# Kernel tuning notes

Hardware: AMD Instinct MI355X
Metric: run time of the kernel (lower is better)

The kernel has to match this reference:

```python
import jax, jax.numpy as jnp
import numpy as np

N_NODES = 10000
N_EDGES = 160000
INPUT_DIM = 24
HIDDEN = 256
Z_DIM = 32
OUT_DIM = 24
HEADS = 2
EW = 2
ENC = HIDDEN + OUT_DIM + 256          # 536
DEC = Z_DIM + HIDDEN + 256            # 544
ENC2 = ENC * HEADS                    # 1072
DEC2 = DEC * HEADS                    # 1088
ENC_MLP_IN = ENC2 + OUT_DIM           # 1096
DEC_MLP_IN = DEC2 + Z_DIM             # 1120


def _lin(key, o, i):
    # kaiming-ish scaling so attention logits stay numerically sane
    return (jax.random.normal(key, (o, i), jnp.float32) / np.sqrt(i)).astype(jnp.float32)


def setup_inputs() -> dict:
    key = jax.random.key(0)
    ks = jax.random.split(key, 32)
    inp = {
        'feats': jax.random.normal(ks[0], (N_NODES, INPUT_DIM), jnp.float32),
        'gt': jax.random.normal(ks[1], (N_NODES, OUT_DIM), jnp.float32),
        'maps_emb': jax.random.normal(ks[2], (N_NODES, 256), jnp.float32),
        'e_w': jax.random.uniform(ks[3], (N_EDGES, EW), jnp.float32),
        'eps': jax.random.normal(ks[4], (N_NODES, Z_DIM), jnp.float32),
        'src': jax.random.randint(ks[5], (N_EDGES,), 0, N_NODES, jnp.int32),
        'dst': jax.random.randint(ks[6], (N_EDGES,), 0, N_NODES, jnp.int32),
        # embedding_h
        'emb_W': _lin(ks[7], HIDDEN, INPUT_DIM),
        'emb_b': jnp.zeros((HIDDEN,), jnp.float32),
        # encoder GAT layer 1 (2 heads, att_ew: Wa covers [z_src|z_dst|ew])
        'enc1_Ws': jnp.stack([_lin(ks[8], ENC, ENC), _lin(ks[9], ENC, ENC)]),
        'enc1_Wf': jnp.stack([_lin(ks[10], ENC, ENC), _lin(ks[11], ENC, ENC)]),
        'enc1_Wa': jnp.stack([_lin(ks[12], 1, 3 * ENC)[0], _lin(ks[13], 1, 3 * ENC)[0]]),
        # encoder GAT layer 2 (1 head, att_ew)
        'enc2_Ws': _lin(ks[14], ENC2, ENC2),
        'enc2_Wf': _lin(ks[15], ENC2, ENC2),
        'enc2_Wa': _lin(ks[16], 1, 3 * ENC2)[0],
        # MLP encoder
        'encmlp_W': _lin(ks[17], ENC_MLP_IN // 2, ENC_MLP_IN),
        'encmlp_b': jnp.zeros((ENC_MLP_IN // 2,), jnp.float32),
        'mu_W': _lin(ks[18], Z_DIM, ENC_MLP_IN // 2),
        'mu_b': jnp.zeros((Z_DIM,), jnp.float32),
        'lv_W': _lin(ks[19], Z_DIM, ENC_MLP_IN // 2),
        'lv_b': jnp.zeros((Z_DIM,), jnp.float32),
        # decoder GAT layer 1 (2 heads, no edge weights in attention)
        'dec1_Ws': jnp.stack([_lin(ks[20], DEC, DEC), _lin(ks[21], DEC, DEC)]),
        'dec1_Wf': jnp.stack([_lin(ks[22], DEC, DEC), _lin(ks[23], DEC, DEC)]),
        'dec1_Wa': jnp.stack([_lin(ks[24], 1, 2 * DEC)[0], _lin(ks[25], 1, 2 * DEC)[0]]),
        # decoder GAT layer 2 (1 head)
        'dec2_Ws': _lin(ks[26], DEC2, DEC2),
        'dec2_Wf': _lin(ks[27], DEC2, DEC2),
        'dec2_Wa': _lin(ks[28], 1, 2 * DEC2)[0],
        # MLP decoder
        'dec0_W': _lin(ks[29], DEC, DEC_MLP_IN),
        'dec0_b': jnp.zeros((DEC,), jnp.float32),
        'dec1o_W': _lin(ks[30], OUT_DIM, DEC),
        'dec1o_b': jnp.zeros((OUT_DIM,), jnp.float32),
    }
    return inp


def rep_pad(ew, pad):
    # nn.ReplicationPad1d(pad): replicate first/last edge-weight column
    left = jnp.repeat(ew[:, :1], pad, axis=1)
    right = jnp.repeat(ew[:, -1:], pad, axis=1)
    return jnp.concatenate([left, ew, right], axis=1)


def gat(h, Ws, Wf, Wa, ew, src, dst, n):
    """One My_GATLayer head: self-lin + gather-attn-softmax-aggregate + relu + residual."""
    out = Ws.shape[0]
    h_s = h @ Ws.T                       # [n, out]
    z = h @ Wf.T                         # [n, out]
    # attention logits without materializing concat([z_src, z_dst, ew])
    logit = (z @ Wa[:out])[src] + (z @ Wa[out:2 * out])[dst]
    if Wa.shape[0] > 2 * out:
        logit = logit + ew @ Wa[2 * out:]
    e = jax.nn.leaky_relu(logit, 0.01)   # [E]
    # per-destination-node edge softmax
    m = jax.ops.segment_max(e, dst, num_segments=n)
    m = jnp.where(jnp.isfinite(m), m, 0.0)
    ex = jnp.exp(e - m[dst])
    s = jax.ops.segment_sum(ex, dst, num_segments=n)
    alpha = ex / s[dst]
    agg = jax.ops.segment_sum(alpha[:, None] * z[src], dst, num_segments=n)
    deg = jax.ops.segment_sum(jnp.ones_like(ex), dst, num_segments=n)
    # DGL: zero-in-degree nodes keep their pre-update ndata['h'] (the input h)
    hn = jnp.where(deg[:, None] > 0, h_s + agg, h)
    return h + jnp.maximum(hn, 0.0)      # relu=True, res_connection=True


def reference(feats, gt, maps_emb, e_w, eps,
              emb_W, emb_b,
              enc1_Ws, enc1_Wf, enc1_Wa, enc2_Ws, enc2_Wf, enc2_Wa,
              encmlp_W, encmlp_b, mu_W, mu_b, lv_W, lv_b,
              dec1_Ws, dec1_Wf, dec1_Wa, dec2_Ws, dec2_Wf, dec2_Wa,
              dec0_W, dec0_b, dec1o_W, dec1o_b,
              src, dst):
    n = feats.shape[0]
    h_emb = feats @ emb_W.T + emb_b
    # ---------------- encoder GAT-VAE ----------------
    h = jnp.concatenate([maps_emb, h_emb, gt], axis=-1)        # [n, ENC]
    e1 = rep_pad(e_w, h.shape[-1] // 2 - 1)                    # [E, ENC]
    h = jnp.concatenate(
        [gat(h, enc1_Ws[i], enc1_Wf[i], enc1_Wa[i], e1, src, dst, n)
         for i in range(enc1_Ws.shape[0])], axis=1)            # [n, ENC*heads]
    e2 = rep_pad(e_w, h.shape[-1] // 2 - 1)                    # [E, ENC*heads]
    h = gat(h, enc2_Ws, enc2_Wf, enc2_Wa, e2, src, dst, n)
    # ---------------- MLP encoder + reparameterize ----------------
    he = jnp.concatenate([h, gt], axis=-1)
    he = jax.nn.leaky_relu(he @ encmlp_W.T + encmlp_b, 0.01)
    mu = he @ mu_W.T + mu_b
    log_var = he @ lv_W.T + lv_b
    z = mu + jnp.exp(0.5 * log_var) * eps
    # ---------------- decoder GAT-VAE (att_ew=False) ----------------
    hd = jnp.concatenate([maps_emb, h_emb, z], axis=-1)        # [n, DEC]
    hd = jnp.concatenate(
        [gat(hd, dec1_Ws[i], dec1_Wf[i], dec1_Wa[i], None, src, dst, n)
         for i in range(dec1_Ws.shape[0])], axis=1)            # [n, DEC*heads]
    hd = gat(hd, dec2_Ws, dec2_Wf, dec2_Wa, None, src, dst, n)
    # ---------------- MLP decoder ----------------
    hd = jnp.concatenate([hd, z], axis=-1)
    hd = jax.nn.leaky_relu(hd @ dec0_W.T + dec0_b, 0.02)
    recon_y = hd @ dec1o_W.T + dec1o_b
    return recon_y
```

## Files before the change

kernel.cpp:

```cpp
#include <hip/hip_runtime.h>
#include <hip/hip_bf16.h>
#include <hip/hip_fp16.h>

#define N_NODES 10000
#define N_EDGES 160000

typedef __attribute__((ext_vector_type(8))) short bf16x8;
typedef __attribute__((ext_vector_type(4))) float f32x4;
typedef __attribute__((ext_vector_type(4))) unsigned short us4v;
typedef unsigned short ushort_t;

__device__ __forceinline__ ushort_t f2bf(float x) {
    union { float f; unsigned u; } c; c.f = x;
    unsigned u = c.u;
    u += 0x7fffu + ((u >> 16) & 1u);
    return (ushort_t)(u >> 16);
}
__device__ __forceinline__ float bf2f(ushort_t b) {
    union { unsigned u; float f; } c; c.u = ((unsigned)b) << 16;
    return c.f;
}
__device__ __forceinline__ ushort_t f2h(float x) {
    return __half_as_ushort(__float2half(x));
}
__device__ __forceinline__ float h2f(ushort_t h) {
    return __half2float(__ushort_as_half(h));
}

__global__ __launch_bounds__(256) void k_split(
    const float* __restrict__ src, int R, int K, int Kp,
    ushort_t* __restrict__ oh, ushort_t* __restrict__ ol, int row_off)
{
    const int q = Kp >> 2;
    const int idx = blockIdx.x * 256 + threadIdx.x;
    if (idx >= R * q) return;
    const int r = idx / q;
    const int k = (idx - r * q) << 2;
    float4 v = make_float4(0.f, 0.f, 0.f, 0.f);
    if (k < K) v = *reinterpret_cast<const float4*>(&src[(size_t)r * K + k]);
    float vv[4] = {v.x, v.y, v.z, v.w};
    us4v h, l;
    #pragma unroll
    for (int j = 0; j < 4; ++j) {
        const ushort_t hb = f2bf(vv[j]);
        h[j] = hb;
        l[j] = f2bf(vv[j] - bf2f(hb));
    }
    const size_t o = (size_t)(r + row_off) * Kp + k;
    *reinterpret_cast<us4v*>(&oh[o]) = h;
    *reinterpret_cast<us4v*>(&ol[o]) = l;
}

__global__ __launch_bounds__(256) void k_mgemm(
    const ushort_t* __restrict__ Ah, const ushort_t* __restrict__ Al,
    const ushort_t* __restrict__ Wh, const ushort_t* __restrict__ Wl,
    const float* __restrict__ bias0, const float* __restrict__ bias1,
    float* __restrict__ C0, int ld0, int M1,
    float* __restrict__ C1, int ld1,
    ushort_t* __restrict__ Z16, int ld16,
    int Nr, int Kp, int Mc, int act, float slope)
{
    __shared__ ushort_t As[128 * 64];
    __shared__ ushort_t Bs[128 * 64];

    const int tid = threadIdx.x;
    const int w = tid >> 6, l = tid & 63;
    const int wr = w >> 1, wc = w & 1;
    const int row0 = blockIdx.y * 128, col0 = blockIdx.x * 128;

    const int rsub = l >> 3;
    const int cg = (((l & 7) ^ (rsub & 7)) << 3);
    const int fr = l & 15, fq = l >> 4;
    const int ca0 = (((0 * 4 + fq) ^ (l & 7)) << 3);
    const int ca1 = (((1 * 4 + fq) ^ (l & 7)) << 3);

    f32x4 acc[4][4];
    #pragma unroll
    for (int m = 0; m < 4; ++m)
        #pragma unroll
        for (int n = 0; n < 4; ++n)
            acc[m][n] = {0.f, 0.f, 0.f, 0.f};

    auto run_seg = [&](const ushort_t* __restrict__ pa,
                       const ushort_t* __restrict__ pb) {
        for (int kt = 0; kt < Kp; kt += 64) {
            #pragma unroll
            for (int i = 0; i < 4; ++i) {
                const int r = w * 32 + i * 8 + rsub;
                int gra = row0 + r; gra = gra < Nr ? gra : Nr - 1;
                const ushort_t* ga = pa + (size_t)gra * Kp + kt + cg;
                __builtin_amdgcn_global_load_lds(
                    (const __attribute__((address_space(1))) void*)ga,
                    (__attribute__((address_space(3))) void*)&As[(w * 32 + i * 8) * 64],
                    16, 0, 0);
                int grb = col0 + r; grb = grb < Mc ? grb : Mc - 1;
                const ushort_t* gb = pb + (size_t)grb * Kp + kt + cg;
                __builtin_amdgcn_global_load_lds(
                    (const __attribute__((address_space(1))) void*)gb,
                    (__attribute__((address_space(3))) void*)&Bs[(w * 32 + i * 8) * 64],
                    16, 0, 0);
            }
            __syncthreads();
            #pragma unroll
            for (int ks = 0; ks < 2; ++ks) {
                const int ca = ks ? ca1 : ca0;
                bf16x8 af[4], bf[4];
                #pragma unroll
                for (int m = 0; m < 4; ++m)
                    af[m] = *reinterpret_cast<const bf16x8*>(
                        &As[(wr * 64 + m * 16 + fr) * 64 + ca]);
                #pragma unroll
                for (int n = 0; n < 4; ++n)
                    bf[n] = *reinterpret_cast<const bf16x8*>(
                        &Bs[(wc * 64 + n * 16 + fr) * 64 + ca]);
                #pragma unroll
                for (int m = 0; m < 4; ++m)
                    #pragma unroll
                    for (int n = 0; n < 4; ++n)
                        acc[m][n] = __builtin_amdgcn_mfma_f32_16x16x32_bf16(
                            af[m], bf[n], acc[m][n], 0, 0, 0);
            }
            __syncthreads();
        }
    };

    run_seg(Ah, Wh);
    run_seg(Ah, Wl);
    run_seg(Al, Wh);

    #pragma unroll
    for (int n = 0; n < 4; ++n) {
        const int col = col0 + wc * 64 + n * 16 + fr;
        if (col >= Mc) continue;
        float bv = 0.f;
        if (col < M1) { if (bias0) bv = bias0[col]; }
        else          { if (bias1) bv = bias1[col - M1]; }
        #pragma unroll
        for (int m = 0; m < 4; ++m) {
            #pragma unroll
            for (int r = 0; r < 4; ++r) {
                const int row = row0 + wr * 64 + m * 16 + fq * 4 + r;
                if (row >= Nr) continue;
                float v = acc[m][n][r] + bv;
                if (act) v = v >= 0.f ? v : v * slope;
                if (col < M1) {
                    if (Z16) Z16[(size_t)row * ld16 + col] = f2h(v);
                    else     C0[(size_t)row * ld0 + col] = v;
                } else {
                    C1[(size_t)row * ld1 + (col - M1)] = v;
                }
            }
        }
    }
}

__global__ void k_hist(const int* __restrict__ dst, int E, int* __restrict__ cnt)
{
    const int e = blockIdx.x * blockDim.x + threadIdx.x;
    if (e < E) atomicAdd(&cnt[dst[e]], 1);
}

__global__ __launch_bounds__(256) void k_scan(const int* __restrict__ cnt,
                                              int* __restrict__ rs, int n)
{
    __shared__ int sums[256];
    const int tid = threadIdx.x;
    const int T = (n + 255) / 256;
    const int base = tid * T;
    int s = 0;
    for (int i = 0; i < T; ++i) { const int idx = base + i; if (idx < n) s += cnt[idx]; }
    sums[tid] = s;
    __syncthreads();
    for (int o = 1; o < 256; o <<= 1) {
        const int v = (tid >= o) ? sums[tid - o] : 0;
        __syncthreads();
        sums[tid] += v;
        __syncthreads();
    }
    int run = (tid == 0) ? 0 : sums[tid - 1];
    for (int i = 0; i < T; ++i) {
        const int idx = base + i;
        if (idx < n) { rs[idx] = run; run += cnt[idx]; }
    }
    if (tid == 255) rs[n] = sums[255];
}

__global__ void k_fill(const int* __restrict__ src, const int* __restrict__ dst,
                       const float* __restrict__ ew, int E,
                       const int* __restrict__ rs, int* __restrict__ cur,
                       int* __restrict__ csrc, float* __restrict__ cew0,
                       float* __restrict__ cew1)
{
    const int e = blockIdx.x * blockDim.x + threadIdx.x;
    if (e >= E) return;
    const int d = dst[e];
    const int pos = rs[d] + atomicAdd(&cur[d], 1);
    csrc[pos] = src[e];
    cew0[pos] = ew[2 * e];
    cew1[pos] = ew[2 * e + 1];
}

__global__ __launch_bounds__(256) void k_dotwa(
    const ushort_t* __restrict__ Z16, const float* __restrict__ wa, int K, int N,
    float* __restrict__ za_s, float* __restrict__ za_d)
{
    const int lane = threadIdx.x & 63;
    const int node = blockIdx.x * 4 + (threadIdx.x >> 6);
    if (node >= N) return;
    const ushort_t* zr = Z16 + (size_t)node * K;
    float s = 0.f, d = 0.f;
    for (int k = lane; k < K; k += 64) {
        const float zv = h2f(zr[k]);
        s += zv * wa[k];
        d += zv * wa[K + k];
    }
    #pragma unroll
    for (int o = 32; o; o >>= 1) { s += __shfl_xor(s, o); d += __shfl_xor(d, o); }
    if (lane == 0) { za_s[node] = s; za_d[node] = d; }
}

__global__ __launch_bounds__(256) void k_wasums(const float* __restrict__ wa,
                                                int out, float* __restrict__ sums)
{
    __shared__ float red[256];
    const int tid = threadIdx.x;
    const int half = out >> 1;
    const float* t0 = wa + 2 * out;
    float s0 = 0.f, s1 = 0.f;
    for (int i = tid; i < half; i += 256) { s0 += t0[i]; s1 += t0[half + i]; }
    red[tid] = s0; __syncthreads();
    for (int o = 128; o; o >>= 1) { if (tid < o) red[tid] += red[tid + o]; __syncthreads(); }
    if (tid == 0) sums[0] = red[0];
    __syncthreads();
    red[tid] = s1; __syncthreads();
    for (int o = 128; o; o >>= 1) { if (tid < o) red[tid] += red[tid + o]; __syncthreads(); }
    if (tid == 0) sums[1] = red[0];
}

__global__ __launch_bounds__(256) void k_attn(
    const int* __restrict__ rs, const int* __restrict__ csrc,
    const float* __restrict__ cew0, const float* __restrict__ cew1,
    const float* __restrict__ za_s, const float* __restrict__ za_d,
    const float* __restrict__ ewsums, float* __restrict__ EV, int N)
{
    const int lane = threadIdx.x & 63;
    const int n = blockIdx.x * 4 + (threadIdx.x >> 6);
    if (n >= N) return;
    const int s0 = rs[n];
    const int cnt = rs[n + 1] - s0;
    if (cnt == 0) return;
    const float zd = za_d[n];
    float w0 = 0.f, w1 = 0.f;
    if (ewsums) { w0 = ewsums[0]; w1 = ewsums[1]; }

    float mx = -INFINITY;
    for (int i = lane; i < cnt; i += 64) {
        float ev = za_s[csrc[s0 + i]] + zd + cew0[s0 + i] * w0 + cew1[s0 + i] * w1;
        ev = ev >= 0.f ? ev : 0.01f * ev;
        EV[s0 + i] = ev;
        mx = fmaxf(mx, ev);
    }
    #pragma unroll
    for (int o = 32; o; o >>= 1) mx = fmaxf(mx, __shfl_xor(mx, o));

    float sum = 0.f;
    for (int i = lane; i < cnt; i += 64) {
        const float ex = expf(EV[s0 + i] - mx);
        EV[s0 + i] = ex;
        sum += ex;
    }
    #pragma unroll
    for (int o = 32; o; o >>= 1) sum += __shfl_xor(sum, o);

    for (int i = lane; i < cnt; i += 64) EV[s0 + i] /= sum;
}

__global__ __launch_bounds__(256) void k_aggfin(
    const int* __restrict__ rs, const int* __restrict__ csrc,
    const float* __restrict__ EV, const ushort_t* __restrict__ Z16,
    const float* __restrict__ HS, const float* __restrict__ Hin,
    float* __restrict__ Out, int N, int out, int ldo, int coff)
{
    const int lane = threadIdx.x & 63;
    const int n = blockIdx.x * 4 + (threadIdx.x >> 6);
    if (n >= N) return;
    const int f = blockIdx.y * 128 + lane * 2;
    if (f >= out) return;
    const int s0 = rs[n];
    const int cnt = rs[n + 1] - s0;

    float ax = 0.f, ay = 0.f, bx = 0.f, by = 0.f;
    int i = 0;
    for (; i + 2 <= cnt; i += 2) {
        const int sn0 = csrc[s0 + i];
        const int sn1 = csrc[s0 + i + 1];
        const float w0 = EV[s0 + i];
        const float w1 = EV[s0 + i + 1];
        union { unsigned u; __half2 h; } c0, c1;
        c0.u = *reinterpret_cast<const unsigned*>(&Z16[(size_t)sn0 * out + f]);
        c1.u = *reinterpret_cast<const unsigned*>(&Z16[(size_t)sn1 * out + f]);
        const float2 z0 = __half22float2(c0.h);
        const float2 z1 = __half22float2(c1.h);
        ax += w0 * z0.x; ay += w0 * z0.y;
        bx += w1 * z1.x; by += w1 * z1.y;
    }
    if (i < cnt) {
        const int sn0 = csrc[s0 + i];
        const float w0 = EV[s0 + i];
        union { unsigned u; __half2 h; } c0;
        c0.u = *reinterpret_cast<const unsigned*>(&Z16[(size_t)sn0 * out + f]);
        const float2 z0 = __half22float2(c0.h);
        ax += w0 * z0.x; ay += w0 * z0.y;
    }
    const float accx = ax + bx, accy = ay + by;

    const float2 hv = *reinterpret_cast<const float2*>(&Hin[(size_t)n * out + f]);
    const float2 hs = *reinterpret_cast<const float2*>(&HS[(size_t)n * out + f]);
    const float hnx = (cnt > 0) ? (hs.x + accx) : hv.x;
    const float hny = (cnt > 0) ? (hs.y + accy) : hv.y;
    float2 o;
    o.x = hv.x + fmaxf(hnx, 0.f);
    o.y = hv.y + fmaxf(hny, 0.f);
    *reinterpret_cast<float2*>(&Out[(size_t)n * ldo + coff + f]) = o;
}

__global__ void k_copy4(const float* __restrict__ src, int s_ld,
                        float* __restrict__ dst, int d_ld, int d_off,
                        int cols, int N)
{
    const int q = cols >> 2;
    const int idx = blockIdx.x * blockDim.x + threadIdx.x;
    if (idx >= N * q) return;
    const int r = idx / q;
    const int c = (idx % q) << 2;
    *reinterpret_cast<float4*>(&dst[(size_t)r * d_ld + d_off + c]) =
        *reinterpret_cast<const float4*>(&src[(size_t)r * s_ld + c]);
}

__global__ void k_reparam(const float* __restrict__ mu, const float* __restrict__ lv,
                          const float* __restrict__ eps, float* __restrict__ z, int total)
{
    const int i = blockIdx.x * blockDim.x + threadIdx.x;
    if (i < total) z[i] = mu[i] + expf(0.5f * lv[i]) * eps[i];
}

static inline void split_mat(hipStream_t st, const float* src, int R, int K, int Kp,
                             ushort_t* oh, ushort_t* ol, int row_off)
{
    const int total = R * (Kp >> 2);
    k_split<<<(total + 255) / 256, 256, 0, st>>>(src, R, K, Kp, oh, ol, row_off);
}

static inline void mgemm(hipStream_t st,
                         const ushort_t* Ah, const ushort_t* Al,
                         const ushort_t* Wh, const ushort_t* Wl,
                         const float* b0, const float* b1,
                         float* C0, int ld0, int M1, float* C1, int ld1,
                         ushort_t* Z16, int ld16,
                         int Nr, int Kp, int Mc, int act, float slope)
{
    dim3 g((Mc + 127) / 128, (Nr + 127) / 128);
    k_mgemm<<<g, 256, 0, st>>>(Ah, Al, Wh, Wl, b0, b1, C0, ld0, M1, C1, ld1,
                               Z16, ld16, Nr, Kp, Mc, act, slope);
}

struct CsrPtrs {
    const int* rs; const int* csrc; const float* cew0; const float* cew1;
};

static void gat_layer(hipStream_t st, const float* Hin, int dim, int Kp,
                      const ushort_t* Ah, const ushort_t* Al,
                      const float* Ws, const float* Wf, const float* Wa, bool has_ew,
                      ushort_t* Wh, ushort_t* Wl,
                      ushort_t* Z16, float* HSb,
                      float* za_s, float* za_d, float* wa_sums,
                      const CsrPtrs& csr, float* EV, float* Out, int ldo, int coff)
{
    split_mat(st, Wf, dim, dim, Kp, Wh, Wl, 0);
    split_mat(st, Ws, dim, dim, Kp, Wh, Wl, dim);
    mgemm(st, Ah, Al, Wh, Wl, nullptr, nullptr,
          nullptr, dim, dim, HSb, dim, Z16, dim, N_NODES, Kp, 2 * dim, 0, 0.f);
    k_dotwa<<<N_NODES / 4, 256, 0, st>>>(Z16, Wa, dim, N_NODES, za_s, za_d);
    const float* es = nullptr;
    if (has_ew) {
        k_wasums<<<1, 256, 0, st>>>(Wa, dim, wa_sums);
        es = wa_sums;
    }
    k_attn<<<N_NODES / 4, 256, 0, st>>>(csr.rs, csr.csrc, csr.cew0, csr.cew1,
                                        za_s, za_d, es, EV, N_NODES);
    dim3 ga(N_NODES / 4, (dim + 127) / 128);
    k_aggfin<<<ga, 256, 0, st>>>(csr.rs, csr.csrc, EV, Z16, HSb, Hin, Out,
                                 N_NODES, dim, ldo, coff);
}

static inline void copy4(hipStream_t st, const float* src, int s_ld,
                         float* dst, int d_ld, int d_off, int cols)
{
    const int total = N_NODES * (cols >> 2);
    k_copy4<<<(total + 255) / 256, 256, 0, st>>>(src, s_ld, dst, d_ld, d_off, cols, N_NODES);
}

extern "C" void kernel_launch(void* const* d_in, const int* in_sizes, int n_in,
                              void* d_out, int out_size, void* d_ws, size_t ws_size,
                              hipStream_t stream)
{
    const float* feats    = (const float*)d_in[0];
    const float* gt       = (const float*)d_in[1];
    const float* maps_emb = (const float*)d_in[2];
    const float* e_w      = (const float*)d_in[3];
    const float* eps      = (const float*)d_in[4];
    const int*   src      = (const int*)d_in[5];
    const int*   dst      = (const int*)d_in[6];
    const float* emb_W    = (const float*)d_in[7];
    const float* emb_b    = (const float*)d_in[8];
    const float* enc1_Ws  = (const float*)d_in[9];
    const float* enc1_Wf  = (const float*)d_in[10];
    const float* enc1_Wa  = (const float*)d_in[11];
    const float* enc2_Ws  = (const float*)d_in[12];
    const float* enc2_Wf  = (const float*)d_in[13];
    const float* enc2_Wa  = (const float*)d_in[14];
    const float* encmlp_W = (const float*)d_in[15];
    const float* encmlp_b = (const float*)d_in[16];
    const float* mu_W     = (const float*)d_in[17];
    const float* mu_b     = (const float*)d_in[18];
    const float* lv_W     = (const float*)d_in[19];
    const float* lv_b     = (const float*)d_in[20];
    const float* dec1_Ws  = (const float*)d_in[21];
    const float* dec1_Wf  = (const float*)d_in[22];
    const float* dec1_Wa  = (const float*)d_in[23];
    const float* dec2_Ws  = (const float*)d_in[24];
    const float* dec2_Wf  = (const float*)d_in[25];
    const float* dec2_Wa  = (const float*)d_in[26];
    const float* dec0_W   = (const float*)d_in[27];
    const float* dec0_b   = (const float*)d_in[28];
    const float* dec1o_W  = (const float*)d_in[29];
    const float* dec1o_b  = (const float*)d_in[30];

    char* wp = (char*)d_ws;
    size_t off = 0;
    auto alloc_f = [&](size_t nf) -> float* {
        float* p = (float*)(wp + off);
        off = (off + nf * sizeof(float) + 255) & ~(size_t)255;
        return p;
    };
    auto alloc_i = [&](size_t ni) -> int* {
        int* p = (int*)(wp + off);
        off = (off + ni * sizeof(int) + 255) & ~(size_t)255;
        return p;
    };
    auto alloc_u = [&](size_t nu) -> ushort_t* {
        ushort_t* p = (ushort_t*)(wp + off);
        off = (off + nu * sizeof(ushort_t) + 255) & ~(size_t)255;
        return p;
    };

    float* A_CAT   = alloc_f((size_t)N_NODES * 1088);
    float* OUTB    = alloc_f((size_t)N_NODES * 1120);
    float* Zb      = alloc_f((size_t)N_NODES * 548);
    float* HSb     = alloc_f((size_t)N_NODES * 1088);
    float* h_emb   = alloc_f((size_t)N_NODES * 256);
    float* zlat    = alloc_f((size_t)N_NODES * 32);
    float* za_s    = alloc_f(N_NODES);
    float* za_d    = alloc_f(N_NODES);
    float* EV      = alloc_f(N_EDGES);
    float* cew0    = alloc_f(N_EDGES);
    float* cew1    = alloc_f(N_EDGES);
    float* wa_sums = alloc_f(64);
    int*   cnt     = alloc_i(N_NODES);
    int*   rs      = alloc_i(N_NODES + 1);
    int*   csrc    = alloc_i(N_EDGES);
    ushort_t* Ah   = alloc_u((size_t)N_NODES * 1152);
    ushort_t* Al   = alloc_u((size_t)N_NODES * 1152);
    ushort_t* Wh   = alloc_u((size_t)2176 * 1088);
    ushort_t* Wl   = alloc_u((size_t)2176 * 1088);
    ushort_t* Z16  = alloc_u((size_t)N_NODES * 1088);
    (void)ws_size; (void)in_sizes; (void)n_in; (void)out_size;

    CsrPtrs csr{rs, csrc, cew0, cew1};

    hipMemsetAsync(cnt, 0, N_NODES * sizeof(int), stream);
    k_hist<<<(N_EDGES + 255) / 256, 256, 0, stream>>>(dst, N_EDGES, cnt);
    k_scan<<<1, 256, 0, stream>>>(cnt, rs, N_NODES);
    hipMemsetAsync(cnt, 0, N_NODES * sizeof(int), stream);
    k_fill<<<(N_EDGES + 255) / 256, 256, 0, stream>>>(src, dst, e_w, N_EDGES,
                                                      rs, cnt, csrc, cew0, cew1);

    split_mat(stream, feats, N_NODES, 24, 64, Ah, Al, 0);
    split_mat(stream, emb_W, 256, 24, 64, Wh, Wl, 0);
    mgemm(stream, Ah, Al, Wh, Wl, emb_b, nullptr,
          h_emb, 256, 256, h_emb, 256, nullptr, 0, N_NODES, 64, 256, 0, 0.f);

    copy4(stream, maps_emb, 256, A_CAT, 536, 0, 256);
    copy4(stream, h_emb, 256, A_CAT, 536, 256, 256);
    copy4(stream, gt, 24, A_CAT, 536, 512, 24);

    split_mat(stream, A_CAT, N_NODES, 536, 576, Ah, Al, 0);
    gat_layer(stream, A_CAT, 536, 576, Ah, Al,
              enc1_Ws, enc1_Wf, enc1_Wa, true, Wh, Wl,
              Z16, HSb, za_s, za_d, wa_sums, csr, EV, OUTB, 1072, 0);
    gat_layer(stream, A_CAT, 536, 576, Ah, Al,
              enc1_Ws + 536 * 536, enc1_Wf + 536 * 536, enc1_Wa + 3 * 536, true,
              Wh, Wl, Z16, HSb, za_s, za_d, wa_sums, csr, EV, OUTB, 1072, 536);

    split_mat(stream, OUTB, N_NODES, 1072, 1088, Ah, Al, 0);
    gat_layer(stream, OUTB, 1072, 1088, Ah, Al,
              enc2_Ws, enc2_Wf, enc2_Wa, true, Wh, Wl,
              Z16, HSb, za_s, za_d, wa_sums, csr, EV, A_CAT, 1072, 0);

    copy4(stream, A_CAT, 1072, OUTB, 1096, 0, 1072);
    copy4(stream, gt, 24, OUTB, 1096, 1072, 24);
    split_mat(stream, OUTB, N_NODES, 1096, 1152, Ah, Al, 0);
    split_mat(stream, encmlp_W, 548, 1096, 1152, Wh, Wl, 0);
    mgemm(stream, Ah, Al, Wh, Wl, encmlp_b, nullptr,
          Zb, 548, 548, Zb, 548, nullptr, 0, N_NODES, 1152, 548, 1, 0.01f);
    float* mu = HSb;
    float* lv = HSb + (size_t)N_NODES * 32;
    split_mat(stream, Zb, N_NODES, 548, 576, Ah, Al, 0);
    split_mat(stream, mu_W, 32, 548, 576, Wh, Wl, 0);
    split_mat(stream, lv_W, 32, 548, 576, Wh, Wl, 32);
    mgemm(stream, Ah, Al, Wh, Wl, mu_b, lv_b,
          mu, 32, 32, lv, 32, nullptr, 0, N_NODES, 576, 64, 0, 0.f);
    k_reparam<<<(N_NODES * 32 + 255) / 256, 256, 0, stream>>>(mu, lv, eps, zlat,
                                                              N_NODES * 32);

    copy4(stream, maps_emb, 256, A_CAT, 544, 0, 256);
    copy4(stream, h_emb, 256, A_CAT, 544, 256, 256);
    copy4(stream, zlat, 32, A_CAT, 544, 512, 32);

    split_mat(stream, A_CAT, N_NODES, 544, 576, Ah, Al, 0);
    gat_layer(stream, A_CAT, 544, 576, Ah, Al,
              dec1_Ws, dec1_Wf, dec1_Wa, false, Wh, Wl,
              Z16, HSb, za_s, za_d, wa_sums, csr, EV, OUTB, 1088, 0);
    gat_layer(stream, A_CAT, 544, 576, Ah, Al,
              dec1_Ws + 544 * 544, dec1_Wf + 544 * 544, dec1_Wa + 2 * 544, false,
              Wh, Wl, Z16, HSb, za_s, za_d, wa_sums, csr, EV, OUTB, 1088, 544);

    split_mat(stream, OUTB, N_NODES, 1088, 1088, Ah, Al, 0);
    gat_layer(stream, OUTB, 1088, 1088, Ah, Al,
              dec2_Ws, dec2_Wf, dec2_Wa, false, Wh, Wl,
              Z16, HSb, za_s, za_d, wa_sums, csr, EV, A_CAT, 1088, 0);

    copy4(stream, A_CAT, 1088, OUTB, 1120, 0, 1088);
    copy4(stream, zlat, 32, OUTB, 1120, 1088, 32);
    split_mat(stream, OUTB, N_NODES, 1120, 1152, Ah, Al, 0);
    split_mat(stream, dec0_W, 544, 1120, 1152, Wh, Wl, 0);
    mgemm(stream, Ah, Al, Wh, Wl, dec0_b, nullptr,
          Zb, 544, 544, Zb, 544, nullptr, 0, N_NODES, 1152, 544, 1, 0.02f);
    split_mat(stream, Zb, N_NODES, 544, 576, Ah, Al, 0);
    split_mat(stream, dec1o_W, 24, 544, 576, Wh, Wl, 0);
    mgemm(stream, Ah, Al, Wh, Wl, dec1o_b, nullptr,
          (float*)d_out, 24, 24, (float*)d_out, 24, nullptr, 0, N_NODES, 576, 24, 0, 0.f);
}
```

Measured before the change: 1.859 ms.

## Fuse split-bf16 GEMM passes into one K loop and batch GAT heads

The three-pass split-bf16 GEMM (hi*hi, hi*lo, lo*hi) now runs in a single K loop. Hi and lo tiles of A and W are loaded together into double LDS buffers, and three MFMAs are issued per fragment pair, so the A/W tiles are read from global memory once instead of three times. Multi-head GAT layers now concatenate all heads' Wf/Ws weights into one wide GEMM, with a new epilogue mode that routes columns to the Z16 or HS buffers with a stride. Downstream kernels gain leading-dimension parameters to match. LDS use doubles to 64 KB per block, which may reduce occupancy.

```diff
diff --git a/kernel.cpp b/kernel.cpp
--- a/kernel.cpp
+++ b/kernel.cpp
@@ -58,10 +58,12 @@
     float* __restrict__ C0, int ld0, int M1,
     float* __restrict__ C1, int ld1,
     ushort_t* __restrict__ Z16, int ld16,
-    int Nr, int Kp, int Mc, int act, float slope)
-{
-    __shared__ ushort_t As[128 * 64];
-    __shared__ ushort_t Bs[128 * 64];
+    int Nr, int Kp, int Mc, int act, float slope, int mode)
+{
+    __shared__ ushort_t As0[128 * 64];
+    __shared__ ushort_t As1[128 * 64];
+    __shared__ ushort_t Bs0[128 * 64];
+    __shared__ ushort_t Bs1[128 * 64];
 
     const int tid = threadIdx.x;
     const int w = tid >> 6, l = tid & 63;
@@ -81,73 +83,94 @@
         for (int n = 0; n < 4; ++n)
             acc[m][n] = {0.f, 0.f, 0.f, 0.f};
 
-    auto run_seg = [&](const ushort_t* __restrict__ pa,
-                       const ushort_t* __restrict__ pb) {
-        for (int kt = 0; kt < Kp; kt += 64) {
+    for (int kt = 0; kt < Kp; kt += 64) {
+        #pragma unroll
+        for (int i = 0; i < 4; ++i) {
+            const int r = w * 32 + i * 8 + rsub;
+            const int lofs = (w * 32 + i * 8) * 64;
+            int gra = row0 + r; gra = gra < Nr ? gra : Nr - 1;
+            const size_t aoff = (size_t)gra * Kp + kt + cg;
+            __builtin_amdgcn_global_load_lds(
+                (const __attribute__((address_space(1))) void*)(Ah + aoff),
+                (__attribute__((address_space(3))) void*)&As0[lofs], 16, 0, 0);
+            __builtin_amdgcn_global_load_lds(
+                (const __attribute__((address_space(1))) void*)(Al + aoff),
+                (__attribute__((address_space(3))) void*)&As1[lofs], 16, 0, 0);
+            int grb = col0 + r; grb = grb < Mc ? grb : Mc - 1;
+            const size_t boff = (size_t)grb * Kp + kt + cg;
+            __builtin_amdgcn_global_load_lds(
+                (const __attribute__((address_space(1))) void*)(Wh + boff),
+                (__attribute__((address_space(3))) void*)&Bs0[lofs], 16, 0, 0);
+            __builtin_amdgcn_global_load_lds(
+                (const __attribute__((address_space(1))) void*)(Wl + boff),
+                (__attribute__((address_space(3))) void*)&Bs1[lofs], 16, 0, 0);
+        }
+        __syncthreads();
+        #pragma unroll
+        for (int ks = 0; ks < 2; ++ks) {
+            const int ca = ks ? ca1 : ca0;
+            bf16x8 ah[4], al4[4], bh[4], bl4[4];
             #pragma unroll
-            for (int i = 0; i < 4; ++i) {
-                const int r = w * 32 + i * 8 + rsub;
-                int gra = row0 + r; gra = gra < Nr ? gra : Nr - 1;
-                const ushort_t* ga = pa + (size_t)gra * Kp + kt + cg;
-                __builtin_amdgcn_global_load_lds(
-                    (const __attribute__((address_space(1))) void*)ga,
-                    (__attribute__((address_space(3))) void*)&As[(w * 32 + i * 8) * 64],
-                    16, 0, 0);
-                int grb = col0 + r; grb = grb < Mc ? grb : Mc - 1;
-                const ushort_t* gb = pb + (size_t)grb * Kp + kt + cg;
-                __builtin_amdgcn_global_load_lds(
-                    (const __attribute__((address_space(1))) void*)gb,
-                    (__attribute__((address_space(3))) void*)&Bs[(w * 32 + i * 8) * 64],
-                    16, 0, 0);
+            for (int m = 0; m < 4; ++m) {
+                const int ro = (wr * 64 + m * 16 + fr) * 64 + ca;
+                ah[m]  = *reinterpret_cast<const bf16x8*>(&As0[ro]);
+                al4[m] = *reinterpret_cast<const bf16x8*>(&As1[ro]);
             }
-            __syncthreads();
             #pragma unroll
-            for (int ks = 0; ks < 2; ++ks) {
-                const int ca = ks ? ca1 : ca0;
-                bf16x8 af[4], bf[4];
+            for (int n = 0; n < 4; ++n) {
+                const int ro = (wc * 64 + n * 16 + fr) * 64 + ca;
+                bh[n]  = *reinterpret_cast<const bf16x8*>(&Bs0[ro]);
+                bl4[n] = *reinterpret_cast<const bf16x8*>(&Bs1[ro]);
+            }
+            #pragma unroll
+            for (int m = 0; m < 4; ++m)
                 #pragma unroll
-                for (int m = 0; m < 4; ++m)
-                    af[m] = *reinterpret_cast<const bf16x8*>(
-                        &As[(wr * 64 + m * 16 + fr) * 64 + ca]);
-                #pragma unroll
-                for (int n = 0; n < 4; ++n)
-                    bf[n] = *reinterpret_cast<const bf16x8*>(
-                        &Bs[(wc * 64 + n * 16 + fr) * 64 + ca]);
-                #pragma unroll
-                for (int m = 0; m < 4; ++m)
-                    #pragma unroll
-                    for (int n = 0; n < 4; ++n)
-                        acc[m][n] = __builtin_amdgcn_mfma_f32_16x16x32_bf16(
-                            af[m], bf[n], acc[m][n], 0, 0, 0);
-            }
-            __syncthreads();
+                for (int n = 0; n < 4; ++n) {
+                    acc[m][n] = __builtin_amdgcn_mfma_f32_16x16x32_bf16(
+                        ah[m], bh[n], acc[m][n], 0, 0, 0);
+                    acc[m][n] = __builtin_amdgcn_mfma_f32_16x16x32_bf16(
+                        ah[m], bl4[n], acc[m][n], 0, 0, 0);
+                    acc[m][n] = __builtin_amdgcn_mfma_f32_16x16x32_bf16(
+                        al4[m], bh[n], acc[m][n], 0, 0, 0);
+                }
         }
-    };
-
-    run_seg(Ah, Wh);
-    run_seg(Ah, Wl);
-    run_seg(Al, Wh);
+        __syncthreads();
+    }
 
     #pragma unroll
     for (int n = 0; n < 4; ++n) {
         const int col = col0 + wc * 64 + n * 16 + fr;
         if (col >= Mc) continue;
-        float bv = 0.f;
-        if (col < M1) { if (bias0) bv = bias0[col]; }
-        else          { if (bias1) bv = bias1[col - M1]; }
-        #pragma unroll
-        for (int m = 0; m < 4; ++m) {
+        if (mode == 0) {
+            float bv = 0.f;
+            if (col < M1) { if (bias0) bv = bias0[col]; }
+            else          { if (bias1) bv = bias1[col - M1]; }
             #pragma unroll
-            for (int r = 0; r < 4; ++r) {
-                const int row = row0 + wr * 64 + m * 16 + fq * 4 + r;
-                if (row >= Nr) continue;
-                float v = acc[m][n][r] + bv;
-                if (act) v = v >= 0.f ? v : v * slope;
-                if (col < M1) {
-                    if (Z16) Z16[(size_t)row * ld16 + col] = f2h(v);
-                    else     C0[(size_t)row * ld0 + col] = v;
-                } else {
-                    C1[(size_t)row * ld1 + (col - M1)] = v;
+            for (int m = 0; m < 4; ++m) {
+                #pragma unroll
+                for (int r = 0; r < 4; ++r) {
+                    const int row = row0 + wr * 64 + m * 16 + fq * 4 + r;
+                    if (row >= Nr) continue;
+                    float v = acc[m][n][r] + bv;
+                    if (act) v = v >= 0.f ? v : v * slope;
+                    if (col < M1) C0[(size_t)row * ld0 + col] = v;
+                    else          C1[(size_t)row * ld1 + (col - M1)] = v;
+                }
+            }
+        } else {
+            const int seg = col / M1;
+            const int rem = col - seg * M1;
+            const int oc = (seg >> 1) * M1 + rem;
+            const bool to_z = (seg & 1) == 0;
+            #pragma unroll
+            for (int m = 0; m < 4; ++m) {
+                #pragma unroll
+                for (int r = 0; r < 4; ++r) {
+                    const int row = row0 + wr * 64 + m * 16 + fq * 4 + r;
+                    if (row >= Nr) continue;
+                    const float v = acc[m][n][r];
+                    if (to_z) Z16[(size_t)row * ld16 + oc] = f2h(v);
+                    else      C1[(size_t)row * ld1 + oc] = v;
                 }
             }
         }
@@ -201,13 +224,14 @@
 }
 
 __global__ __launch_bounds__(256) void k_dotwa(
-    const ushort_t* __restrict__ Z16, const float* __restrict__ wa, int K, int N,
+    const ushort_t* __restrict__ Z16, int ldz,
+    const float* __restrict__ wa, int K, int N,
     float* __restrict__ za_s, float* __restrict__ za_d)
 {
     const int lane = threadIdx.x & 63;
     const int node = blockIdx.x * 4 + (threadIdx.x >> 6);
     if (node >= N) return;
-    const ushort_t* zr = Z16 + (size_t)node * K;
+    const ushort_t* zr = Z16 + (size_t)node * ldz;
     float s = 0.f, d = 0.f;
     for (int k = lane; k < K; k += 64) {
         const float zv = h2f(zr[k]);
@@ -277,8 +301,9 @@
 
 __global__ __launch_bounds__(256) void k_aggfin(
     const int* __restrict__ rs, const int* __restrict__ csrc,
-    const float* __restrict__ EV, const ushort_t* __restrict__ Z16,
-    const float* __restrict__ HS, const float* __restrict__ Hin,
+    const float* __restrict__ EV, const ushort_t* __restrict__ Z16, int ldz,
+    const float* __restrict__ HS, int ldh,
+    const float* __restrict__ Hin, int ldi,
     float* __restrict__ Out, int N, int out, int ldo, int coff)
 {
     const int lane = threadIdx.x & 63;
@@ -297,8 +322,8 @@
         const float w0 = EV[s0 + i];
         const float w1 = EV[s0 + i + 1];
         union { unsigned u; __half2 h; } c0, c1;
-        c0.u = *reinterpret_cast<const unsigned*>(&Z16[(size_t)sn0 * out + f]);
-        c1.u = *reinterpret_cast<const unsigned*>(&Z16[(size_t)sn1 * out + f]);
+        c0.u = *reinterpret_cast<const unsigned*>(&Z16[(size_t)sn0 * ldz + f]);
+        c1.u = *reinterpret_cast<const unsigned*>(&Z16[(size_t)sn1 * ldz + f]);
         const float2 z0 = __half22float2(c0.h);
         const float2 z1 = __half22float2(c1.h);
         ax += w0 * z0.x; ay += w0 * z0.y;
@@ -308,14 +333,14 @@
         const int sn0 = csrc[s0 + i];
         const float w0 = EV[s0 + i];
         union { unsigned u; __half2 h; } c0;
-        c0.u = *reinterpret_cast<const unsigned*>(&Z16[(size_t)sn0 * out + f]);
+        c0.u = *reinterpret_cast<const unsigned*>(&Z16[(size_t)sn0 * ldz + f]);
         const float2 z0 = __half22float2(c0.h);
         ax += w0 * z0.x; ay += w0 * z0.y;
     }
     const float accx = ax + bx, accy = ay + by;
 
-    const float2 hv = *reinterpret_cast<const float2*>(&Hin[(size_t)n * out + f]);
-    const float2 hs = *reinterpret_cast<const float2*>(&HS[(size_t)n * out + f]);
+    const float2 hv = *reinterpret_cast<const float2*>(&Hin[(size_t)n * ldi + f]);
+    const float2 hs = *reinterpret_cast<const float2*>(&HS[(size_t)n * ldh + f]);
     const float hnx = (cnt > 0) ? (hs.x + accx) : hv.x;
     const float hny = (cnt > 0) ? (hs.y + accy) : hv.y;
     float2 o;
@@ -357,40 +382,49 @@
                          const float* b0, const float* b1,
                          float* C0, int ld0, int M1, float* C1, int ld1,
                          ushort_t* Z16, int ld16,
-                         int Nr, int Kp, int Mc, int act, float slope)
+                         int Nr, int Kp, int Mc, int act, float slope, int mode)
 {
     dim3 g((Mc + 127) / 128, (Nr + 127) / 128);
     k_mgemm<<<g, 256, 0, st>>>(Ah, Al, Wh, Wl, b0, b1, C0, ld0, M1, C1, ld1,
-                               Z16, ld16, Nr, Kp, Mc, act, slope);
+                               Z16, ld16, Nr, Kp, Mc, act, slope, mode);
 }
 
 struct CsrPtrs {
     const int* rs; const int* csrc; const float* cew0; const float* cew1;
 };
 
-static void gat_layer(hipStream_t st, const float* Hin, int dim, int Kp,
+static void gat_layer(hipStream_t st, const float* Hin, int dim, int Kp, int nheads,
                       const ushort_t* Ah, const ushort_t* Al,
-                      const float* Ws, const float* Wf, const float* Wa, bool has_ew,
+                      const float* const* Ws, const float* const* Wf,
+                      const float* const* Wa, bool has_ew,
                       ushort_t* Wh, ushort_t* Wl,
                       ushort_t* Z16, float* HSb,
                       float* za_s, float* za_d, float* wa_sums,
-                      const CsrPtrs& csr, float* EV, float* Out, int ldo, int coff)
-{
-    split_mat(st, Wf, dim, dim, Kp, Wh, Wl, 0);
-    split_mat(st, Ws, dim, dim, Kp, Wh, Wl, dim);
+                      const CsrPtrs& csr, float* EV, float* Out, int ldo)
+{
+    for (int h = 0; h < nheads; ++h) {
+        split_mat(st, Wf[h], dim, dim, Kp, Wh, Wl, (2 * h) * dim);
+        split_mat(st, Ws[h], dim, dim, Kp, Wh, Wl, (2 * h + 1) * dim);
+    }
+    const int ldz = nheads * dim;
     mgemm(st, Ah, Al, Wh, Wl, nullptr, nullptr,
-          nullptr, dim, dim, HSb, dim, Z16, dim, N_NODES, Kp, 2 * dim, 0, 0.f);
-    k_dotwa<<<N_NODES / 4, 256, 0, st>>>(Z16, Wa, dim, N_NODES, za_s, za_d);
-    const float* es = nullptr;
-    if (has_ew) {
-        k_wasums<<<1, 256, 0, st>>>(Wa, dim, wa_sums);
-        es = wa_sums;
-    }
-    k_attn<<<N_NODES / 4, 256, 0, st>>>(csr.rs, csr.csrc, csr.cew0, csr.cew1,
-                                        za_s, za_d, es, EV, N_NODES);
-    dim3 ga(N_NODES / 4, (dim + 127) / 128);
-    k_aggfin<<<ga, 256, 0, st>>>(csr.rs, csr.csrc, EV, Z16, HSb, Hin, Out,
-                                 N_NODES, dim, ldo, coff);
+          nullptr, 0, dim, HSb, ldz, Z16, ldz,
+          N_NODES, Kp, 2 * nheads * dim, 0, 0.f, 1);
+    for (int h = 0; h < nheads; ++h) {
+        k_dotwa<<<N_NODES / 4, 256, 0, st>>>(Z16 + h * dim, ldz, Wa[h], dim,
+                                             N_NODES, za_s, za_d);
+        const float* es = nullptr;
+        if (has_ew) {
+            k_wasums<<<1, 256, 0, st>>>(Wa[h], dim, wa_sums);
+            es = wa_sums;
+        }
+        k_attn<<<N_NODES / 4, 256, 0, st>>>(csr.rs, csr.csrc, csr.cew0, csr.cew1,
+                                            za_s, za_d, es, EV, N_NODES);
+        dim3 ga(N_NODES / 4, (dim + 127) / 128);
+        k_aggfin<<<ga, 256, 0, st>>>(csr.rs, csr.csrc, EV,
+                                     Z16 + h * dim, ldz, HSb + h * dim, ldz,
+                                     Hin, dim, Out, N_NODES, dim, ldo, h * dim);
+    }
 }
 
 static inline void copy4(hipStream_t st, const float* src, int s_ld,
@@ -488,38 +522,43 @@
     split_mat(stream, feats, N_NODES, 24, 64, Ah, Al, 0);
     split_mat(stream, emb_W, 256, 24, 64, Wh, Wl, 0);
     mgemm(stream, Ah, Al, Wh, Wl, emb_b, nullptr,
-          h_emb, 256, 256, h_emb, 256, nullptr, 0, N_NODES, 64, 256, 0, 0.f);
+          h_emb, 256, 256, h_emb, 256, nullptr, 0, N_NODES, 64, 256, 0, 0.f, 0);
 
     copy4(stream, maps_emb, 256, A_CAT, 536, 0, 256);
     copy4(stream, h_emb, 256, A_CAT, 536, 256, 256);
     copy4(stream, gt, 24, A_CAT, 536, 512, 24);
 
     split_mat(stream, A_CAT, N_NODES, 536, 576, Ah, Al, 0);
-    gat_layer(stream, A_CAT, 536, 576, Ah, Al,
-              enc1_Ws, enc1_Wf, enc1_Wa, true, Wh, Wl,
-              Z16, HSb, za_s, za_d, wa_sums, csr, EV, OUTB, 1072, 0);
-    gat_layer(stream, A_CAT, 536, 576, Ah, Al,
-              enc1_Ws + 536 * 536, enc1_Wf + 536 * 536, enc1_Wa + 3 * 536, true,
-              Wh, Wl, Z16, HSb, za_s, za_d, wa_sums, csr, EV, OUTB, 1072, 536);
+    {
+        const float* Wsv[2] = {enc1_Ws, enc1_Ws + 536 * 536};
+        const float* Wfv[2] = {enc1_Wf, enc1_Wf + 536 * 536};
+        const float* Wav[2] = {enc1_Wa, enc1_Wa + 3 * 536};
+        gat_layer(stream, A_CAT, 536, 576, 2, Ah, Al, Wsv, Wfv, Wav, true,
+                  Wh, Wl, Z16, HSb, za_s, za_d, wa_sums, csr, EV, OUTB, 1072);
+    }
 
     split_mat(stream, OUTB, N_NODES, 1072, 1088, Ah, Al, 0);
-    gat_layer(stream, OUTB, 1072, 1088, Ah, Al,
-              enc2_Ws, enc2_Wf, enc2_Wa, true, Wh, Wl,
-              Z16, HSb, za_s, za_d, wa_sums, csr, EV, A_CAT, 1072, 0);
+    {
+        const float* Wsv[1] = {enc2_Ws};
+        const float* Wfv[1] = {enc2_Wf};
+        const float* Wav[1] = {enc2_Wa};
+        gat_layer(stream, OUTB, 1072, 1088, 1, Ah, Al, Wsv, Wfv, Wav, true,
+                  Wh, Wl, Z16, HSb, za_s, za_d, wa_sums, csr, EV, A_CAT, 1072);
+    }
 
     copy4(stream, A_CAT, 1072, OUTB, 1096, 0, 1072);
     copy4(stream, gt, 24, OUTB, 1096, 1072, 24);
     split_mat(stream, OUTB, N_NODES, 1096, 1152, Ah, Al, 0);
     split_mat(stream, encmlp_W, 548, 1096, 1152, Wh, Wl, 0);
     mgemm(stream, Ah, Al, Wh, Wl, encmlp_b, nullptr,
-          Zb, 548, 548, Zb, 548, nullptr, 0, N_NODES, 1152, 548, 1, 0.01f);
+          Zb, 548, 548, Zb, 548, nullptr, 0, N_NODES, 1152, 548, 1, 0.01f, 0);
     float* mu = HSb;
     float* lv = HSb + (size_t)N_NODES * 32;
     split_mat(stream, Zb, N_NODES, 548, 576, Ah, Al, 0);
     split_mat(stream, mu_W, 32, 548, 576, Wh, Wl, 0);
     split_mat(stream, lv_W, 32, 548, 576, Wh, Wl, 32);
     mgemm(stream, Ah, Al, Wh, Wl, mu_b, lv_b,
-          mu, 32, 32, lv, 32, nullptr, 0, N_NODES, 576, 64, 0, 0.f);
+          mu, 32, 32, lv, 32, nullptr, 0, N_NODES, 576, 64, 0, 0.f, 0);
     k_reparam<<<(N_NODES * 32 + 255) / 256, 256, 0, stream>>>(mu, lv, eps, zlat,
                                                               N_NODES * 32);
 
@@ -528,26 +567,31 @@
     copy4(stream, zlat, 32, A_CAT, 544, 512, 32);
 
     split_mat(stream, A_CAT, N_NODES, 544, 576, Ah, Al, 0);
-    gat_layer(stream, A_CAT, 544, 576, Ah, Al,
-              dec1_Ws, dec1_Wf, dec1_Wa, false, Wh, Wl,
-              Z16, HSb, za_s, za_d, wa_sums, csr, EV, OUTB, 1088, 0);
-    gat_layer(stream, A_CAT, 544, 576, Ah, Al,
-              dec1_Ws + 544 * 544, dec1_Wf + 544 * 544, dec1_Wa + 2 * 544, false,
-              Wh, Wl, Z16, HSb, za_s, za_d, wa_sums, csr, EV, OUTB, 1088, 544);
+    {
+        const float* Wsv[2] = {dec1_Ws, dec1_Ws + 544 * 544};
+        const float* Wfv[2] = {dec1_Wf, dec1_Wf + 544 * 544};
+        const float* Wav[2] = {dec1_Wa, dec1_Wa + 2 * 544};
+        gat_layer(stream, A_CAT, 544, 576, 2, Ah, Al, Wsv, Wfv, Wav, false,
+                  Wh, Wl, Z16, HSb, za_s, za_d, wa_sums, csr, EV, OUTB, 1088);
+    }
 
     split_mat(stream, OUTB, N_NODES, 1088, 1088, Ah, Al, 0);
-    gat_layer(stream, OUTB, 1088, 1088, Ah, Al,
-              dec2_Ws, dec2_Wf, dec2_Wa, false, Wh, Wl,
-              Z16, HSb, za_s, za_d, wa_sums, csr, EV, A_CAT, 1088, 0);
+    {
+        const float* Wsv[1] = {dec2_Ws};
+        const float* Wfv[1] = {dec2_Wf};
+        const float* Wav[1] = {dec2_Wa};
+        gat_layer(stream, OUTB, 1088, 1088, 1, Ah, Al, Wsv, Wfv, Wav, false,
+                  Wh, Wl, Z16, HSb, za_s, za_d, wa_sums, csr, EV, A_CAT, 1088);
+    }
 
     copy4(stream, A_CAT, 1088, OUTB, 1120, 0, 1088);
     copy4(stream, zlat, 32, OUTB, 1120, 1088, 32);
     split_mat(stream, OUTB, N_NODES, 1120, 1152, Ah, Al, 0);
     split_mat(stream, dec0_W, 544, 1120, 1152, Wh, Wl, 0);
     mgemm(stream, Ah, Al, Wh, Wl, dec0_b, nullptr,
-          Zb, 544, 544, Zb, 544, nullptr, 0, N_NODES, 1152, 544, 1, 0.02f);
+          Zb, 544, 544, Zb, 544, nullptr, 0, N_NODES, 1152, 544, 1, 0.02f, 0);
     split_mat(stream, Zb, N_NODES, 544, 576, Ah, Al, 0);
     split_mat(stream, dec1o_W, 24, 544, 576, Wh, Wl, 0);
     mgemm(stream, Ah, Al, Wh, Wl, dec1o_b, nullptr,
-          (float*)d_out, 24, 24, (float*)d_out, 24, nullptr, 0, N_NODES, 576, 24, 0, 0.f);
-}
+          (float*)d_out, 24, 24, (float*)d_out, 24, nullptr, 0, N_NODES, 576, 24, 0, 0.f, 0);
+}
```

Measured after the change: 1.534 ms. 1.21x faster.
